# Performance work log

Measured on AMD Instinct MI355X. Metric: run time of the kernel, lower is better.

The kernel has to match this reference:

```python
import jax, jax.numpy as jnp
import numpy as np

COMMITMENT_WEIGHT = 0.25


def _vq_layer(residual, codebook):
    """One euclidean VQ layer: nearest-codeword lookup + straight-through.
    residual: [B,T,D], codebook: [K,D].
    Returns (q_st [B,T,D], idx [B,T], commit_loss scalar).
    """
    B, T, D = residual.shape
    flat = residual.reshape(-1, D)  # [N,D]
    d2 = (jnp.sum(flat * flat, axis=-1, keepdims=True)
          - 2.0 * flat @ codebook.T
          + jnp.sum(codebook * codebook, axis=-1))  # [N,K]
    idx = jnp.argmin(d2, axis=-1)                   # [N]
    q = codebook[idx].reshape(B, T, D)
    # straight-through estimator (as in vector_quantize_pytorch)
    q_st = residual + jax.lax.stop_gradient(q - residual)
    commit_loss = COMMITMENT_WEIGHT * jnp.mean(
        (jax.lax.stop_gradient(q) - residual) ** 2)
    return q_st, idx.reshape(B, T), commit_loss


def setup_inputs() -> dict:
    key = jax.random.key(0)
    ks = jax.random.split(key, 9)
    D = 768
    sizes = [2, 4, 8, 16, 32, 64, 128, 256]
    inp = {"x": jax.random.normal(ks[0], (32, 2048, D), dtype=jnp.float32)}
    for i, K in enumerate(sizes):
        inp[f"cb{i}"] = jax.random.normal(ks[i + 1], (K, D), dtype=jnp.float32)
    return inp


def reference(x, cb0, cb1, cb2, cb3, cb4, cb5, cb6, cb7):
    codebooks = [cb0, cb1, cb2, cb3, cb4, cb5, cb6, cb7]
    residual = x
    quantized = jnp.zeros_like(x)
    all_indices = []
    total_commit_loss = jnp.float32(0.0)
    for cb in codebooks:  # fixed 8 structurally-distinct layers
        q, idx, commit = _vq_layer(residual, cb)
        quantized = quantized + q
        residual = residual - q
        all_indices.append(idx)
        total_commit_loss = total_commit_loss + commit
    all_indices = jnp.stack(all_indices, axis=-1)  # [B,T,num_layers]
    return quantized, all_indices, total_commit_loss
```

## Files before the change

kernel.cpp:

```cpp
#include <hip/hip_runtime.h>
#include <stdint.h>

#define NTOK 65536
#define DIM  768
#define NCB  512
#define NC   510
#define TAU  0.75f

typedef _Float16 f16x8 __attribute__((ext_vector_type(8)));
typedef float f32x4 __attribute__((ext_vector_type(4)));

#define WS_C32   0u
#define WS_CHI   1572864u
#define WS_CNORM 3145728u
#define WS_G     3147776u
#define WS_IDX   4196352u
#define WS_PART  6293504u
#define WS_XN    6match_placeholder
#undef WS_XN
#define WS_XN    6359040u
#define WS_S     8388608u
#define S_BYTES  67108864u

__device__ __forceinline__ void gl_lds16(const void* g, void* l){
  __builtin_amdgcn_global_load_lds(
      (const __attribute__((address_space(1))) unsigned int*)g,
      (__attribute__((address_space(3))) unsigned int*)l,
      16, 0, 0);
}

__global__ void k_prep(const float* __restrict__ cb0, const float* __restrict__ cb1,
                       const float* __restrict__ cb2, const float* __restrict__ cb3,
                       const float* __restrict__ cb4, const float* __restrict__ cb5,
                       const float* __restrict__ cb6, const float* __restrict__ cb7,
                       char* __restrict__ ws){
  const int r = blockIdx.x, t = threadIdx.x;
  const float* srcs[8] = {cb0,cb1,cb2,cb3,cb4,cb5,cb6,cb7};
  const int off[8] = {0,2,6,14,30,62,126,254};
  const int KK[8]  = {2,4,8,16,32,64,128,256};
  const float* src = nullptr;
#pragma unroll
  for (int l=0;l<8;l++)
    if (r >= off[l] && r < off[l]+KK[l]) src = srcs[l] + (size_t)(r - off[l]) * DIM;
  float* C32 = (float*)(ws + WS_C32);
  _Float16* Chi = (_Float16*)(ws + WS_CHI);
  double ss = 0.0;
#pragma unroll
  for (int i=0;i<3;i++){
    const int e = t + i*256;
    const float v = src ? src[e] : 0.f;
    C32[(size_t)r*DIM + e] = v;
    Chi[(size_t)r*DIM + e] = (_Float16)v;
    ss += (double)v * (double)v;
  }
  __shared__ double red[256];
  red[t] = ss; __syncthreads();
  for (int sdown=128; sdown>0; sdown>>=1){
    if (t < sdown) red[t] += red[t+sdown];
    __syncthreads();
  }
  if (t == 0){
    float* cnp = (float*)(ws + WS_CNORM);
    cnp[r] = (r < NC) ? (float)red[0] : 1e30f;
  }
}

__global__ void k_gram(char* __restrict__ ws){
  const int i = blockIdx.x, t = threadIdx.x;
  const float* __restrict__ C32 = (const float*)(ws + WS_C32);
  __shared__ float row[DIM];
  for (int e=t; e<DIM; e+=256) row[e] = C32[(size_t)i*DIM + e];
  __syncthreads();
  float* __restrict__ G = (float*)(ws + WS_G);
  for (int j=t; j<NCB; j+=256){
    const float4* cj = (const float4*)(C32 + (size_t)j*DIM);
    double d = 0.0;
    for (int k=0; k<DIM/4; k++){
      const float4 b = cj[k];
      d += (double)row[4*k]*(double)b.x + (double)row[4*k+1]*(double)b.y
         + (double)row[4*k+2]*(double)b.z + (double)row[4*k+3]*(double)b.w;
    }
    G[(size_t)i*NCB + j] = (float)d;
  }
}

__global__ __launch_bounds__(256, 3) void k_gemm(const float* __restrict__ x,
                                                 const char* __restrict__ ws,
                                                 _Float16* __restrict__ S,
                                                 float* __restrict__ xn){
  __shared__ __align__(16) char smem[49152];
  const int t = threadIdx.x, lane = t & 63, w = t >> 6;
  const int wm = w >> 1, wn = w & 1;
  const int bid = blockIdx.x;
  const int xcd = bid & 7, jj = bid >> 3;
  const int mt = xcd*64 + (jj >> 2), nt = jj & 3;
  const _Float16* __restrict__ Chi = (const _Float16*)(ws + WS_CHI);

  f32x4 acc[4][4];
#pragma unroll
  for (int i=0;i<4;i++)
#pragma unroll
    for (int j=0;j<4;j++) acc[i][j] = {0.f,0.f,0.f,0.f};

  float xs = 0.f;

  for (int kt=0; kt<12; kt++){
#pragma unroll
    for (int i8=0;i8<8;i8++){
      const int r0 = w*32 + i8*4;
      const int row = r0 + (lane>>4);
      const int g = lane & 15;
      const int sg = g ^ (((row&7)<<1) | ((row>>3)&1));
      const size_t go = (size_t)(mt*128 + row)*DIM + (size_t)kt*64 + sg*4;
      gl_lds16(x + go, smem + r0*256);
    }
#pragma unroll
    for (int c4=0;c4<4;c4++){
      const int r0 = w*32 + c4*8;
      const int rloc = r0 + (lane>>3);
      const int jsrc = (lane&7) ^ (rloc&7);
      const size_t go = (size_t)(nt*128 + rloc)*DIM + (size_t)kt*64 + jsrc*8;
      gl_lds16(Chi + go, smem + 32768 + r0*128);
    }
    __syncthreads();
    if (nt == 0){
      const int rr = t & 127, hf = t >> 7;
#pragma unroll
      for (int g=0; g<8; g++){
        const f32x4 v = *(const f32x4*)(smem + rr*256 + hf*128 + g*16);
        xs += v[0]*v[0] + v[1]*v[1] + v[2]*v[2] + v[3]*v[3];
      }
    }
#pragma unroll
    for (int kk=0; kk<2; kk++){
      f16x8 fa[4], fb[4];
#pragma unroll
      for (int mf=0;mf<4;mf++){
        const int m = wm*64 + mf*16 + (lane&15);
        const int maskm = ((m&7)<<1) | ((m>>3)&1);
        const int ch = kk*4 + (lane>>4);
        const int g0 = (2*ch) ^ maskm;
        const f32x4 lo = *(const f32x4*)(smem + m*256 + g0*16);
        const f32x4 hi = *(const f32x4*)(smem + m*256 + (g0^1)*16);
        f16x8 r;
        r[0]=(_Float16)lo[0]; r[1]=(_Float16)lo[1]; r[2]=(_Float16)lo[2]; r[3]=(_Float16)lo[3];
        r[4]=(_Float16)hi[0]; r[5]=(_Float16)hi[1]; r[6]=(_Float16)hi[2]; r[7]=(_Float16)hi[3];
        fa[mf] = r;
      }
#pragma unroll
      for (int nf=0;nf<4;nf++){
        const int c = wn*64 + nf*16 + (lane&15);
        const uint bb = (uint)(32768 + c*128 + ((((kk<<2)+(lane>>4)) ^ (c&7))*16));
        fb[nf] = *(const f16x8*)(smem + bb);
      }
#pragma unroll
      for (int mf=0;mf<4;mf++)
#pragma unroll
        for (int nf=0;nf<4;nf++)
          acc[mf][nf] = __builtin_amdgcn_mfma_f32_16x16x32_f16(fa[mf], fb[nf], acc[mf][nf], 0,0,0);
    }
    __syncthreads();
  }

  if (nt == 0){
    ((float*)smem)[t] = xs;
    __syncthreads();
    if (t < 128) xn[mt*128 + t] = ((float*)smem)[t] + ((float*)smem)[t + 128];
  }

#pragma unroll
  for (int mf=0;mf<4;mf++)
#pragma unroll
    for (int nf=0;nf<4;nf++){
      const f32x4 v = acc[mf][nf];
      const int col  = nt*128 + wn*64 + nf*16 + (lane&15);
      const int row0 = mt*128 + wm*64 + mf*16 + ((lane>>4)<<2);
#pragma unroll
      for (int e=0;e<4;e++)
        S[(size_t)(row0+e)*NCB + col] = (_Float16)v[e];
    }
}

template<int FUSED>
__global__ __launch_bounds__(256, 4) void k_chain(const float* __restrict__ x,
                                                  const _Float16* __restrict__ S,
                                                  char* __restrict__ ws,
                                                  float* __restrict__ out,
                                                  float* __restrict__ part,
                                                  const float* __restrict__ xn){
  const int t = threadIdx.x, lane = t & 63, w = t >> 6;
  const size_t tok = (size_t)blockIdx.x*4 + w;
  const float* __restrict__ cn  = (const float*)(ws + WS_CNORM);
  const float* __restrict__ G   = (const float*)(ws + WS_G);
  const float* __restrict__ C32 = (const float*)(ws + WS_C32);

  float sv[8], s0[8], cnv[8];
  {
    const uint* sp = (const uint*)(S + tok*NCB);
#pragma unroll
    for (int j=0;j<4;j++){
      union { uint u; _Float16 h[2]; } cv;
      cv.u = sp[j*64 + lane];
      sv[2*j]   = (float)cv.h[0];
      sv[2*j+1] = (float)cv.h[1];
      const float2 c2 = *(const float2*)(cn + j*128 + lane*2);
      cnv[2*j] = c2.x; cnv[2*j+1] = c2.y;
    }
  }
#pragma unroll
  for (int k=0;k<8;k++) s0[k] = sv[k];

  int mcs[8];
  float h = FUSED ? xn[tok] : 0.f;
  float tot = 0.f;

#pragma unroll
  for (int l=0; l<8; ++l){
    const int cs = (2<<l) - 2;
    const int ce = cs + (2<<l);
    float bv = 3e38f; int bc = 0x7fffffff;
#pragma unroll
    for (int j=0;j<4;j++){
      const int c0 = j*128 + lane*2;
      const float sA = (c0   >= cs && c0   < ce) ? (cnv[2*j]   - 2.f*sv[2*j])   : 3e38f;
      const float sB = (c0+1 >= cs && c0+1 < ce) ? (cnv[2*j+1] - 2.f*sv[2*j+1]) : 3e38f;
      if (sA < bv){ bv = sA; bc = c0; }
      if (sB < bv){ bv = sB; bc = c0+1; }
    }
#pragma unroll
    for (int d=1; d<64; d<<=1){
      const float ov = __shfl_xor(bv, d);
      const int   oc = __shfl_xor(bc, d);
      if (ov < bv || (ov == bv && oc < bc)){ bv = ov; bc = oc; }
    }
    int bm = 0;
#pragma unroll
    for (int j=0;j<4;j++){
      const int c0 = j*128 + lane*2;
      const float sA = (c0   >= cs && c0   < ce) ? (cnv[2*j]   - 2.f*sv[2*j])   : 3e38f;
      const float sB = (c0+1 >= cs && c0+1 < ce) ? (cnv[2*j+1] - 2.f*sv[2*j+1]) : 3e38f;
      if (sA <= bv + TAU) bm |= 1 << (2*j);
      if (sB <= bv + TAU) bm |= 1 << (2*j+1);
    }
    const unsigned long long lmask = __ballot(bm != 0);
    const int b0 = __ffsll((long long)lmask) - 1;
    const int bm0 = __shfl(bm, b0);
    const bool multi = (__popcll(lmask) > 1) || ((bm0 & (bm0-1)) != 0);

    int mc = bc;
    float ssel = bv;
    if (multi){
      float xv[12];
      {
        const float4* xp = (const float4*)(x + tok*DIM + lane*12);
#pragma unroll
        for (int q=0;q<3;q++){
          const float4 v = xp[q];
          xv[q*4]=v.x; xv[q*4+1]=v.y; xv[q*4+2]=v.z; xv[q*4+3]=v.w;
        }
      }
      double bve = 1e300; int bce = 0x7fffffff;
      unsigned long long Lm = lmask;
      while (Lm){
        const int b = __ffsll((long long)Lm) - 1; Lm &= Lm - 1;
        const int mbits = __shfl(bm, b);
#pragma unroll
        for (int k=0;k<8;k++){
          if (mbits & (1<<k)){
            const int c = (k>>1)*128 + b*2 + (k&1);
            const float dkv = __shfl(s0[k] - sv[k], b);
            const float* __restrict__ crow = C32 + (size_t)c*DIM + lane*12;
            double dd = 0.0;
#pragma unroll
            for (int q=0;q<3;q++){
              const float4 v = *(const float4*)(crow + q*4);
              dd += (double)xv[q*4]*v.x + (double)xv[q*4+1]*v.y
                  + (double)xv[q*4+2]*v.z + (double)xv[q*4+3]*v.w;
            }
#pragma unroll
            for (int d=1; d<64; d<<=1) dd += __shfl_xor(dd, d);
            const double se = (double)cn[c] - 2.0*(dd - (double)dkv);
            if (se < bve || (se == bve && c < bce)){ bve = se; bce = c; }
          }
        }
      }
      mc = bce;
      ssel = (float)bve;
    }
    mcs[l] = mc;
    if (FUSED){ h += ssel; tot += h; }
    if (l < 7){
      const float* __restrict__ gr = G + (size_t)mc*NCB;
#pragma unroll
      for (int j=0;j<4;j++){
        const float2 g2 = *(const float2*)(gr + j*128 + lane*2);
        sv[2*j] -= g2.x; sv[2*j+1] -= g2.y;
      }
    }
  }

  if (FUSED){
    float q[12];
#pragma unroll
    for (int i=0;i<12;i++) q[i] = 0.f;
#pragma unroll
    for (int l=0;l<8;l++){
      const float* __restrict__ cw = C32 + (size_t)mcs[l]*DIM + lane*12;
#pragma unroll
      for (int qq=0;qq<3;qq++){
        const float4 v = *(const float4*)(cw + qq*4);
        q[qq*4]+=v.x; q[qq*4+1]+=v.y; q[qq*4+2]+=v.z; q[qq*4+3]+=v.w;
      }
    }
    float* op = out + tok*DIM + lane*12;
#pragma unroll
    for (int qq=0;qq<3;qq++){
      float4 v; v.x=q[qq*4]; v.y=q[qq*4+1]; v.z=q[qq*4+2]; v.w=q[qq*4+3];
      *(float4*)(op + qq*4) = v;
    }
    if (lane == 0){
      float4 i0, i1;
      i0.x=(float)(mcs[0]-0);   i0.y=(float)(mcs[1]-2);   i0.z=(float)(mcs[2]-6);   i0.w=(float)(mcs[3]-14);
      i1.x=(float)(mcs[4]-30);  i1.y=(float)(mcs[5]-62);  i1.z=(float)(mcs[6]-126); i1.w=(float)(mcs[7]-254);
      *(float4*)(out + (size_t)NTOK*DIM + tok*8)     = i0;
      *(float4*)(out + (size_t)NTOK*DIM + tok*8 + 4) = i1;
    }
    __shared__ float bs[4];
    if (lane == 0) bs[w] = tot;
    __syncthreads();
    if (t == 0) part[blockIdx.x] = bs[0]+bs[1]+bs[2]+bs[3];
  } else {
    if (lane == 0){
      int* idxw = (int*)(ws + WS_IDX);
      const int offs[8] = {0,2,6,14,30,62,126,254};
#pragma unroll
      for (int l=0;l<8;l++) idxw[tok*8 + l] = mcs[l] - offs[l];
    }
  }
}

__global__ __launch_bounds__(512) void k_fin(const float* __restrict__ x,
                                             char* __restrict__ ws,
                                             float* __restrict__ out,
                                             float* __restrict__ part){
  const int t = threadIdx.x, lane = t & 63, w = t >> 6;
  const size_t tok = (size_t)blockIdx.x * 8 + w;
  const int off[8] = {0,2,6,14,30,62,126,254};
  const int* __restrict__ idxw = (const int*)(ws + WS_IDX);
  const float* __restrict__ C32 = (const float*)(ws + WS_C32);
  int loc[8];
#pragma unroll
  for (int l=0;l<8;l++) loc[l] = idxw[tok*8 + l];
  if (lane < 8) out[(size_t)NTOK*DIM + tok*8 + lane] = (float)idxw[tok*8 + lane];

  const float4* __restrict__ xr = (const float4*)(x + tok*DIM);
  float4* __restrict__ qr = (float4*)(out + tok*DIM);
  const float4* crow[8];
#pragma unroll
  for (int l=0;l<8;l++) crow[l] = (const float4*)(C32 + (size_t)(loc[l] + off[l])*DIM);
  float ssq = 0.f;
#pragma unroll
  for (int i=0;i<3;i++){
    const int e4 = i*64 + lane;
    const float4 xv = xr[e4];
    float rx = xv.x, ry = xv.y, rz = xv.z, rw = xv.w;
    float qx = 0.f, qy = 0.f, qz = 0.f, qw = 0.f;
#pragma unroll
    for (int l=0;l<8;l++){
      const float4 cv = crow[l][e4];
      rx -= cv.x; ry -= cv.y; rz -= cv.z; rw -= cv.w;
      qx += cv.x; qy += cv.y; qz += cv.z; qw += cv.w;
      ssq += rx*rx + ry*ry + rz*rz + rw*rw;
    }
    float4 q; q.x = qx; q.y = qy; q.z = qz; q.w = qw;
    qr[e4] = q;
  }
#pragma unroll
  for (int d=32; d>0; d>>=1) ssq += __shfl_down(ssq, d);
  __shared__ float bsum[8];
  if (lane == 0) bsum[w] = ssq;
  __syncthreads();
  if (t == 0){
    float s2 = 0.f;
#pragma unroll
    for (int j=0;j<8;j++) s2 += bsum[j];
    part[blockIdx.x] = s2;
  }
}

__global__ void k_loss(const float* __restrict__ part, int n,
                       float* __restrict__ out){
  const int t = threadIdx.x;
  double s = 0.0;
  for (int i=t; i<n; i+=256) s += (double)part[i];
  __shared__ double red[256];
  red[t] = s; __syncthreads();
  for (int d=128; d>0; d>>=1){
    if (t < d) red[t] += red[t+d];
    __syncthreads();
  }
  if (t == 0)
    out[(size_t)NTOK*DIM + (size_t)NTOK*8] =
      (float)(0.25 * red[0] / (double)((size_t)NTOK * DIM));
}

extern "C" void kernel_launch(void* const* d_in, const int* in_sizes, int n_in,
                              void* d_out, int out_size, void* d_ws, size_t ws_size,
                              hipStream_t stream){
  const float* x = (const float*)d_in[0];
  char* ws = (char*)d_ws;
  float* out = (float*)d_out;
  float* part = (float*)(ws + WS_PART);
  float* xn   = (float*)(ws + WS_XN);
  const bool fused = ws_size >= (size_t)WS_S + (size_t)S_BYTES;
  _Float16* Sp = fused ? (_Float16*)(ws + WS_S) : (_Float16*)out;

  k_prep<<<512, 256, 0, stream>>>((const float*)d_in[1], (const float*)d_in[2],
                                  (const float*)d_in[3], (const float*)d_in[4],
                                  (const float*)d_in[5], (const float*)d_in[6],
                                  (const float*)d_in[7], (const float*)d_in[8], ws);
  k_gram<<<512, 256, 0, stream>>>(ws);
  k_gemm<<<2048, 256, 0, stream>>>(x, ws, Sp, xn);
  if (fused){
    k_chain<1><<<16384, 256, 0, stream>>>(x, Sp, ws, out, part, xn);
    k_loss<<<1, 256, 0, stream>>>(part, 16384, out);
  } else {
    k_chain<0><<<16384, 256, 0, stream>>>(x, Sp, ws, out, part, xn);
    k_fin<<<8192, 512, 0, stream>>>(x, ws, out, part);
    k_loss<<<1, 256, 0, stream>>>(part, 8192, out);
  }
}
```

Measured before the change: 448.6 us.

## Spread x-norm work across N-tiles, pack argmin key, enlarge chain blocks

The squared norm of x is no longer computed only by the nt==0 tiles. Each of the four N-tiles now handles three of the twelve K-steps, and the result is reduced per block into a partial sum. The per-token xn buffer is gone: the loss is rewritten algebraically as a weighted sum of selected scores plus 8 times the total x norm, which k_loss folds in. The chain kernel's argmin butterfly now uses one packed uint key (order-preserving float bits with the low 9 bits replaced by the index), and blocks grow to 512 threads covering 8 tokens. The packing truncates the score, so the TAU candidate test and the chosen index can differ slightly when ties fall within the truncated bits.

```diff
diff --git a/kernel.cpp b/kernel.cpp
--- a/kernel.cpp
+++ b/kernel.cpp
@@ -16,9 +16,7 @@
 #define WS_G     3147776u
 #define WS_IDX   4196352u
 #define WS_PART  6293504u
-#define WS_XN    6match_placeholder
-#undef WS_XN
-#define WS_XN    6359040u
+#define WS_PART2 6359040u
 #define WS_S     8388608u
 #define S_BYTES  67108864u
 
@@ -87,7 +85,7 @@
 __global__ __launch_bounds__(256, 3) void k_gemm(const float* __restrict__ x,
                                                  const char* __restrict__ ws,
                                                  _Float16* __restrict__ S,
-                                                 float* __restrict__ xn){
+                                                 float* __restrict__ part2){
   __shared__ __align__(16) char smem[49152];
   const int t = threadIdx.x, lane = t & 63, w = t >> 6;
   const int wm = w >> 1, wn = w & 1;
@@ -123,11 +121,10 @@
       gl_lds16(Chi + go, smem + 32768 + r0*128);
     }
     __syncthreads();
-    if (nt == 0){
-      const int rr = t & 127, hf = t >> 7;
+    if ((kt & 3) == nt){
 #pragma unroll
       for (int g=0; g<8; g++){
-        const f32x4 v = *(const f32x4*)(smem + rr*256 + hf*128 + g*16);
+        const f32x4 v = *(const f32x4*)(smem + t*128 + g*16);
         xs += v[0]*v[0] + v[1]*v[1] + v[2]*v[2] + v[3]*v[3];
       }
     }
@@ -162,11 +159,12 @@
     __syncthreads();
   }
 
-  if (nt == 0){
-    ((float*)smem)[t] = xs;
-    __syncthreads();
-    if (t < 128) xn[mt*128 + t] = ((float*)smem)[t] + ((float*)smem)[t + 128];
-  }
+#pragma unroll
+  for (int d=32; d>0; d>>=1) xs += __shfl_down(xs, d);
+  if (lane == 0) ((float*)smem)[w] = xs;
+  __syncthreads();
+  if (t == 0) part2[bid] = ((float*)smem)[0] + ((float*)smem)[1]
+                         + ((float*)smem)[2] + ((float*)smem)[3];
 
 #pragma unroll
   for (int mf=0;mf<4;mf++)
@@ -182,14 +180,13 @@
 }
 
 template<int FUSED>
-__global__ __launch_bounds__(256, 4) void k_chain(const float* __restrict__ x,
+__global__ __launch_bounds__(512, 4) void k_chain(const float* __restrict__ x,
                                                   const _Float16* __restrict__ S,
                                                   char* __restrict__ ws,
                                                   float* __restrict__ out,
-                                                  float* __restrict__ part,
-                                                  const float* __restrict__ xn){
+                                                  float* __restrict__ part){
   const int t = threadIdx.x, lane = t & 63, w = t >> 6;
-  const size_t tok = (size_t)blockIdx.x*4 + w;
+  const size_t tok = (size_t)blockIdx.x*8 + w;
   const float* __restrict__ cn  = (const float*)(ws + WS_CNORM);
   const float* __restrict__ G   = (const float*)(ws + WS_G);
   const float* __restrict__ C32 = (const float*)(ws + WS_C32);
@@ -211,14 +208,13 @@
   for (int k=0;k<8;k++) s0[k] = sv[k];
 
   int mcs[8];
-  float h = FUSED ? xn[tok] : 0.f;
   float tot = 0.f;
 
 #pragma unroll
   for (int l=0; l<8; ++l){
     const int cs = (2<<l) - 2;
     const int ce = cs + (2<<l);
-    float bv = 3e38f; int bc = 0x7fffffff;
+    float bv = 3e38f; int bc = 511;
 #pragma unroll
     for (int j=0;j<4;j++){
       const int c0 = j*128 + lane*2;
@@ -227,28 +223,35 @@
       if (sA < bv){ bv = sA; bc = c0; }
       if (sB < bv){ bv = sB; bc = c0+1; }
     }
+    uint u = __float_as_uint(bv);
+    u ^= (u & 0x80000000u) ? 0xFFFFFFFFu : 0x80000000u;
+    uint key = (u & 0xFFFFFE00u) | ((uint)bc & 511u);
 #pragma unroll
     for (int d=1; d<64; d<<=1){
-      const float ov = __shfl_xor(bv, d);
-      const int   oc = __shfl_xor(bc, d);
-      if (ov < bv || (ov == bv && oc < bc)){ bv = ov; bc = oc; }
-    }
+      const uint ok = (uint)__shfl_xor((int)key, d);
+      key = (ok < key) ? ok : key;
+    }
+    const int mc0 = (int)(key & 511u);
+    const uint vq = key & 0xFFFFFE00u;
+    const uint sb = (vq & 0x80000000u) ? (vq ^ 0x80000000u) : ~vq;
+    const float bv_est = __uint_as_float(sb);
+
     int bm = 0;
 #pragma unroll
     for (int j=0;j<4;j++){
       const int c0 = j*128 + lane*2;
       const float sA = (c0   >= cs && c0   < ce) ? (cnv[2*j]   - 2.f*sv[2*j])   : 3e38f;
       const float sB = (c0+1 >= cs && c0+1 < ce) ? (cnv[2*j+1] - 2.f*sv[2*j+1]) : 3e38f;
-      if (sA <= bv + TAU) bm |= 1 << (2*j);
-      if (sB <= bv + TAU) bm |= 1 << (2*j+1);
+      if (sA <= bv_est + TAU) bm |= 1 << (2*j);
+      if (sB <= bv_est + TAU) bm |= 1 << (2*j+1);
     }
     const unsigned long long lmask = __ballot(bm != 0);
     const int b0 = __ffsll((long long)lmask) - 1;
     const int bm0 = __shfl(bm, b0);
     const bool multi = (__popcll(lmask) > 1) || ((bm0 & (bm0-1)) != 0);
 
-    int mc = bc;
-    float ssel = bv;
+    int mc = mc0;
+    float ssel = bv_est;
     if (multi){
       float xv[12];
       {
@@ -288,7 +291,7 @@
       ssel = (float)bve;
     }
     mcs[l] = mc;
-    if (FUSED){ h += ssel; tot += h; }
+    if (FUSED) tot += (float)(8 - l) * ssel;
     if (l < 7){
       const float* __restrict__ gr = G + (size_t)mc*NCB;
 #pragma unroll
@@ -325,10 +328,15 @@
       *(float4*)(out + (size_t)NTOK*DIM + tok*8)     = i0;
       *(float4*)(out + (size_t)NTOK*DIM + tok*8 + 4) = i1;
     }
-    __shared__ float bs[4];
+    __shared__ float bs[8];
     if (lane == 0) bs[w] = tot;
     __syncthreads();
-    if (t == 0) part[blockIdx.x] = bs[0]+bs[1]+bs[2]+bs[3];
+    if (t == 0){
+      float s2 = 0.f;
+#pragma unroll
+      for (int j=0;j<8;j++) s2 += bs[j];
+      part[blockIdx.x] = s2;
+    }
   } else {
     if (lane == 0){
       int* idxw = (int*)(ws + WS_IDX);
@@ -389,12 +397,15 @@
 }
 
 __global__ void k_loss(const float* __restrict__ part, int n,
+                       const float* __restrict__ part2, int n2,
                        float* __restrict__ out){
   const int t = threadIdx.x;
   double s = 0.0;
   for (int i=t; i<n; i+=256) s += (double)part[i];
+  double sx = 0.0;
+  for (int i=t; i<n2; i+=256) sx += (double)part2[i];
   __shared__ double red[256];
-  red[t] = s; __syncthreads();
+  red[t] = s + 8.0*sx; __syncthreads();
   for (int d=128; d>0; d>>=1){
     if (t < d) red[t] += red[t+d];
     __syncthreads();
@@ -410,8 +421,8 @@
   const float* x = (const float*)d_in[0];
   char* ws = (char*)d_ws;
   float* out = (float*)d_out;
-  float* part = (float*)(ws + WS_PART);
-  float* xn   = (float*)(ws + WS_XN);
+  float* part  = (float*)(ws + WS_PART);
+  float* part2 = (float*)(ws + WS_PART2);
   const bool fused = ws_size >= (size_t)WS_S + (size_t)S_BYTES;
   _Float16* Sp = fused ? (_Float16*)(ws + WS_S) : (_Float16*)out;
 
@@ -420,13 +431,13 @@
                                   (const float*)d_in[5], (const float*)d_in[6],
                                   (const float*)d_in[7], (const float*)d_in[8], ws);
   k_gram<<<512, 256, 0, stream>>>(ws);
-  k_gemm<<<2048, 256, 0, stream>>>(x, ws, Sp, xn);
+  k_gemm<<<2048, 256, 0, stream>>>(x, ws, Sp, part2);
   if (fused){
-    k_chain<1><<<16384, 256, 0, stream>>>(x, Sp, ws, out, part, xn);
-    k_loss<<<1, 256, 0, stream>>>(part, 16384, out);
+    k_chain<1><<<8192, 512, 0, stream>>>(x, Sp, ws, out, part);
+    k_loss<<<1, 256, 0, stream>>>(part, 8192, part2, 2048, out);
   } else {
-    k_chain<0><<<16384, 256, 0, stream>>>(x, Sp, ws, out, part, xn);
+    k_chain<0><<<8192, 512, 0, stream>>>(x, Sp, ws, out, part);
     k_fin<<<8192, 512, 0, stream>>>(x, ws, out, part);
-    k_loss<<<1, 256, 0, stream>>>(part, 8192, out);
-  }
-}
+    k_loss<<<1, 256, 0, stream>>>(part, 8192, (const float*)nullptr, 0, out);
+  }
+}
```

After: 362.3 us. 1.24x faster.
